# Kernel tuning notes

Hardware: AMD Instinct MI355X
Metric: run time of the kernel (lower is better)

## Reference

```python
import jax, jax.numpy as jnp
import numpy as np

# Normalizer hyperparameters (from init_kwargs)
THETA = 0.3     # final temperature theta
THETA0 = 4.0    # initial annealing temperature
T = 20          # number of annealing iterations
BETA = 0.7      # temperature decay
P = 0.1         # fraction -> k = p * (# finite entries per row)
TEMPERATURE = 1.0

BSZ, SEQ = 4096, 8192


def setup_inputs() -> dict:
    key = jax.random.key(0)
    k1, k2 = jax.random.split(key)
    score = jax.random.normal(k1, (BSZ, SEQ), dtype=jnp.float32)
    mask = jax.random.randint(k2, (BSZ, SEQ), 0, 2, dtype=jnp.int32)
    return {"score": score, "mask": mask}


def reference(score, mask):
    # score: [bsz, seq], mask: [bsz, seq] (0 = masked out)
    score = score * TEMPERATURE
    score = jnp.where(mask == 0, -jnp.inf, score)

    # k = p * number of finite (unmasked) entries per row
    k = jnp.sum(jnp.isfinite(score), axis=-1, keepdims=True).astype(score.dtype) * P

    # annealed temperature schedule: theta_t = max(beta^t * theta0, theta)
    thetas = [max(BETA ** t * THETA0, THETA) for t in range(T)]

    a = jnp.zeros((score.shape[0], 1), dtype=score.dtype)
    b = jnp.zeros_like(score)
    for th in thetas:
        # masked entries: exp(-inf)=0, relu(-inf)=0 -> they contribute nothing
        s = jnp.sum(jnp.exp((score + b) / th), axis=-1, keepdims=True)  # [bsz,1]
        a = th * jnp.log(k / (s + 1e-20))                               # [bsz,1]
        b = -jax.nn.relu(score + a)                                     # [bsz,seq]

    gamma = jnp.exp((score + a + b) / THETA)  # [bsz, seq]
    return gamma
```

## Files before the change

### kernel.cpp

```cpp
#include <hip/hip_runtime.h>
#include <math.h>

#define SEQ   8192
#define NT    64
#define VPT   128
#define F4PT  32

__device__ __forceinline__ float wave_sum(float x) {
    #pragma unroll
    for (int off = 32; off > 0; off >>= 1)
        x += __shfl_xor(x, off, 64);
    return x;
}

__global__ __launch_bounds__(NT) void normalizer_kernel(
        const float* __restrict__ score,
        const int*   __restrict__ mask,
        float*       __restrict__ out)
{
    const int row  = blockIdx.x;
    const int lane = threadIdx.x;

    constexpr double L2E = 1.4426950408889634;
    constexpr double TH7 = 4.0*0.7*0.7*0.7*0.7*0.7*0.7*0.7;
    const float cu0 = (float)(L2E / 4.0);
    const float r07 = (float)(1.0 / 0.7);
    const float ce  = (float)(TH7 / 0.3);

    const float4* __restrict__ s4 = (const float4*)(score + (size_t)row * SEQ);
    const int4*   __restrict__ m4 = (const int4*)(mask  + (size_t)row * SEQ);

    float u[VPT];
    int cnt = 0;
    #pragma unroll
    for (int j = 0; j < F4PT; ++j) {
        float4 s = s4[j * NT + lane];
        int4   m = m4[j * NT + lane];
        u[4*j+0] = m.x ? s.x * cu0 : -INFINITY;
        u[4*j+1] = m.y ? s.y * cu0 : -INFINITY;
        u[4*j+2] = m.z ? s.z * cu0 : -INFINITY;
        u[4*j+3] = m.w ? s.w * cu0 : -INFINITY;
        cnt += (m.x != 0) + (m.y != 0) + (m.z != 0) + (m.w != 0);
    }

    float a0 = 0.f, a1 = 0.f, a2 = 0.f, a3 = 0.f;
    #pragma unroll
    for (int j = 0; j < VPT; j += 4) {
        a0 += __builtin_amdgcn_exp2f(u[j]);
        a1 += __builtin_amdgcn_exp2f(u[j+1]);
        a2 += __builtin_amdgcn_exp2f(u[j+2]);
        a3 += __builtin_amdgcn_exp2f(u[j+3]);
    }
    float s_ = wave_sum((a0 + a1) + (a2 + a3));
    float kf = 0.1f * wave_sum((float)cnt);
    #pragma unroll
    for (int j = 0; j < VPT; ++j) u[j] *= r07;
    const float l2k = __builtin_amdgcn_logf(kf);
    const float rk  = 1.0f / kf;
    float NAcp = (__builtin_amdgcn_logf(s_ + 1e-20f) - l2k) * r07;

    for (int t = 1; t < 7; ++t) {
        a0 = 0.f; a1 = 0.f; a2 = 0.f; a3 = 0.f;
        #pragma unroll
        for (int j = 0; j < VPT; j += 4) {
            a0 += __builtin_amdgcn_exp2f(fminf(u[j],   NAcp));
            a1 += __builtin_amdgcn_exp2f(fminf(u[j+1], NAcp));
            a2 += __builtin_amdgcn_exp2f(fminf(u[j+2], NAcp));
            a3 += __builtin_amdgcn_exp2f(fminf(u[j+3], NAcp));
        }
        #pragma unroll
        for (int j = 0; j < VPT; ++j) u[j] *= r07;
        float ss = wave_sum((a0 + a1) + (a2 + a3));
        NAcp = (__builtin_amdgcn_logf(ss + 1e-20f) - l2k) * r07;
    }

    float eNA;
    {
        a0 = 0.f; a1 = 0.f; a2 = 0.f; a3 = 0.f;
        #pragma unroll
        for (int j = 0; j < VPT; j += 4) {
            a0 += __builtin_amdgcn_exp2f(fminf(u[j],   NAcp));
            a1 += __builtin_amdgcn_exp2f(fminf(u[j+1], NAcp));
            a2 += __builtin_amdgcn_exp2f(fminf(u[j+2], NAcp));
            a3 += __builtin_amdgcn_exp2f(fminf(u[j+3], NAcp));
        }
        #pragma unroll
        for (int j = 0; j < VPT; ++j)
            u[j] = __builtin_amdgcn_exp2f(u[j] * ce);
        float ss = wave_sum((a0 + a1) + (a2 + a3));
        eNA = __builtin_amdgcn_exp2f((__builtin_amdgcn_logf(ss + 1e-20f) - l2k) * ce);
    }

    for (int t = 8; t < 20; ++t) {
        a0 = 0.f; a1 = 0.f; a2 = 0.f; a3 = 0.f;
        #pragma unroll
        for (int j = 0; j < VPT; j += 4) {
            a0 += fminf(u[j],   eNA);
            a1 += fminf(u[j+1], eNA);
            a2 += fminf(u[j+2], eNA);
            a3 += fminf(u[j+3], eNA);
        }
        float ss = wave_sum((a0 + a1) + (a2 + a3));
        eNA = (ss + 1e-20f) * rk;
    }

    const float ra = 1.0f / eNA;
    float4* __restrict__ o4 = (float4*)(out + (size_t)row * SEQ);
    #pragma unroll
    for (int j = 0; j < F4PT; ++j) {
        float4 g;
        g.x = fminf(u[4*j+0], eNA) * ra;
        g.y = fminf(u[4*j+1], eNA) * ra;
        g.z = fminf(u[4*j+2], eNA) * ra;
        g.w = fminf(u[4*j+3], eNA) * ra;
        o4[j * NT + lane] = g;
    }
}

extern "C" void kernel_launch(void* const* d_in, const int* in_sizes, int n_in,
                              void* d_out, int out_size, void* d_ws, size_t ws_size,
                              hipStream_t stream) {
    const float* score = (const float*)d_in[0];
    const int*   mask  = (const int*)d_in[1];
    float*       out   = (float*)d_out;
    const int rows = in_sizes[0] / SEQ;
    normalizer_kernel<<<rows, NT, 0, stream>>>(score, mask, out);
}
```

Before: 367.7 us.

## Split each row across four wavefronts with shared-memory cross-wave reductions

Each row now goes to a 256-thread block of four wavefronts instead of a single wavefront. Each thread holds 32 values instead of 128, which cuts register pressure and raises occupancy. Per-iteration sums are reduced inside each wave, then combined across waves through double-buffered shared memory and a block barrier. This adds 20 __syncthreads per row in exchange for more latency hiding and less register spilling risk.

```diff
diff --git a/kernel.cpp b/kernel.cpp
--- a/kernel.cpp
+++ b/kernel.cpp
@@ -2,9 +2,9 @@
 #include <math.h>
 
 #define SEQ   8192
-#define NT    64
-#define VPT   128
-#define F4PT  32
+#define NT    256
+#define VPT   32
+#define F4PT  8
 
 __device__ __forceinline__ float wave_sum(float x) {
     #pragma unroll
@@ -19,7 +19,9 @@
         float*       __restrict__ out)
 {
     const int row  = blockIdx.x;
-    const int lane = threadIdx.x;
+    const int tid  = threadIdx.x;
+    const int wid  = tid >> 6;
+    const int lane = tid & 63;
 
     constexpr double L2E = 1.4426950408889634;
     constexpr double TH7 = 4.0*0.7*0.7*0.7*0.7*0.7*0.7*0.7;
@@ -34,14 +36,17 @@
     int cnt = 0;
     #pragma unroll
     for (int j = 0; j < F4PT; ++j) {
-        float4 s = s4[j * NT + lane];
-        int4   m = m4[j * NT + lane];
+        float4 s = s4[j * NT + tid];
+        int4   m = m4[j * NT + tid];
         u[4*j+0] = m.x ? s.x * cu0 : -INFINITY;
         u[4*j+1] = m.y ? s.y * cu0 : -INFINITY;
         u[4*j+2] = m.z ? s.z * cu0 : -INFINITY;
         u[4*j+3] = m.w ? s.w * cu0 : -INFINITY;
         cnt += (m.x != 0) + (m.y != 0) + (m.z != 0) + (m.w != 0);
     }
+
+    __shared__ float redc[4];
+    __shared__ float red[2][4];
 
     float a0 = 0.f, a1 = 0.f, a2 = 0.f, a3 = 0.f;
     #pragma unroll
@@ -51,12 +56,16 @@
         a2 += __builtin_amdgcn_exp2f(u[j+2]);
         a3 += __builtin_amdgcn_exp2f(u[j+3]);
     }
-    float s_ = wave_sum((a0 + a1) + (a2 + a3));
-    float kf = 0.1f * wave_sum((float)cnt);
+    float pc = wave_sum((float)cnt);
+    float ps = wave_sum((a0 + a1) + (a2 + a3));
+    if (lane == 0) { redc[wid] = pc; red[0][wid] = ps; }
     #pragma unroll
     for (int j = 0; j < VPT; ++j) u[j] *= r07;
+    __syncthreads();
+    const float kf  = 0.1f * (redc[0] + redc[1] + redc[2] + redc[3]);
     const float l2k = __builtin_amdgcn_logf(kf);
     const float rk  = 1.0f / kf;
+    float s_ = red[0][0] + red[0][1] + red[0][2] + red[0][3];
     float NAcp = (__builtin_amdgcn_logf(s_ + 1e-20f) - l2k) * r07;
 
     for (int t = 1; t < 7; ++t) {
@@ -68,10 +77,13 @@
             a2 += __builtin_amdgcn_exp2f(fminf(u[j+2], NAcp));
             a3 += __builtin_amdgcn_exp2f(fminf(u[j+3], NAcp));
         }
+        float pa = wave_sum((a0 + a1) + (a2 + a3));
+        if (lane == 0) red[t & 1][wid] = pa;
         #pragma unroll
         for (int j = 0; j < VPT; ++j) u[j] *= r07;
-        float ss = wave_sum((a0 + a1) + (a2 + a3));
-        NAcp = (__builtin_amdgcn_logf(ss + 1e-20f) - l2k) * r07;
+        __syncthreads();
+        s_ = red[t & 1][0] + red[t & 1][1] + red[t & 1][2] + red[t & 1][3];
+        NAcp = (__builtin_amdgcn_logf(s_ + 1e-20f) - l2k) * r07;
     }
 
     float eNA;
@@ -84,11 +96,14 @@
             a2 += __builtin_amdgcn_exp2f(fminf(u[j+2], NAcp));
             a3 += __builtin_amdgcn_exp2f(fminf(u[j+3], NAcp));
         }
+        float pa = wave_sum((a0 + a1) + (a2 + a3));
+        if (lane == 0) red[1][wid] = pa;
         #pragma unroll
         for (int j = 0; j < VPT; ++j)
             u[j] = __builtin_amdgcn_exp2f(u[j] * ce);
-        float ss = wave_sum((a0 + a1) + (a2 + a3));
-        eNA = __builtin_amdgcn_exp2f((__builtin_amdgcn_logf(ss + 1e-20f) - l2k) * ce);
+        __syncthreads();
+        s_ = red[1][0] + red[1][1] + red[1][2] + red[1][3];
+        eNA = __builtin_amdgcn_exp2f((__builtin_amdgcn_logf(s_ + 1e-20f) - l2k) * ce);
     }
 
     for (int t = 8; t < 20; ++t) {
@@ -100,8 +115,11 @@
             a2 += fminf(u[j+2], eNA);
             a3 += fminf(u[j+3], eNA);
         }
-        float ss = wave_sum((a0 + a1) + (a2 + a3));
-        eNA = (ss + 1e-20f) * rk;
+        float pa = wave_sum((a0 + a1) + (a2 + a3));
+        if (lane == 0) red[t & 1][wid] = pa;
+        __syncthreads();
+        s_ = red[t & 1][0] + red[t & 1][1] + red[t & 1][2] + red[t & 1][3];
+        eNA = (s_ + 1e-20f) * rk;
     }
 
     const float ra = 1.0f / eNA;
@@ -113,7 +131,7 @@
         g.y = fminf(u[4*j+1], eNA) * ra;
         g.z = fminf(u[4*j+2], eNA) * ra;
         g.w = fminf(u[4*j+3], eNA) * ra;
-        o4[j * NT + lane] = g;
+        o4[j * NT + tid] = g;
     }
 }
 
```

New measurement: 326.0 us. 1.13x faster.
